# Kernel tuning notes

Measured on AMD Instinct MI355X. Metric: run time of the kernel, lower is better.

The kernel has to match this reference:

```python
import jax, jax.numpy as jnp
import numpy as np
import math

NUM_HEADS = 4
PH, PW = 8, 8

def setup_inputs() -> dict:
    key = jax.random.key(0)
    ks = jax.random.split(key, 12)
    B, C, H, W = 2, 128, 256, 256
    x = jax.random.normal(ks[0], (B, C, H, W), dtype=jnp.float32)
    mask = jax.random.uniform(ks[1], (B, 1, H, W), dtype=jnp.float32)
    s1 = 1.0 / math.sqrt(C)          # kaiming-ish scale for 1x1 convs
    s3 = 1.0 / math.sqrt(C * 9)      # 3x3 conv
    wq = jax.random.normal(ks[2], (C, C), dtype=jnp.float32) * s1
    bq = jax.random.normal(ks[3], (C,), dtype=jnp.float32) * 0.01
    wk = jax.random.normal(ks[4], (C, C), dtype=jnp.float32) * s1
    bk = jax.random.normal(ks[5], (C,), dtype=jnp.float32) * 0.01
    wv = jax.random.normal(ks[6], (C, C), dtype=jnp.float32) * s1
    bv = jax.random.normal(ks[7], (C,), dtype=jnp.float32) * 0.01
    wo = jax.random.normal(ks[8], (C, C, 3, 3), dtype=jnp.float32) * s3
    bo = jax.random.normal(ks[9], (C,), dtype=jnp.float32) * 0.01
    return {"x": x, "mask": mask, "wq": wq, "bq": bq, "wk": wk, "bk": bk,
            "wv": wv, "bv": bv, "wo": wo, "bo": bo}

def _conv1x1(x, w, b):
    # w: [O, I]; x: [B, C, H, W]
    return jnp.einsum('oc,bchw->bohw', w, x) + b[None, :, None, None]

def _window(t, b, heads, dph, out_h, out_w):
    # [B, C, H, W] -> [B, heads, out_h*out_w, dph*PH*PW]
    t = t.reshape(b, heads, dph, out_h, PH, out_w, PW)
    t = t.transpose(0, 1, 3, 5, 2, 4, 6)
    return t.reshape(b, heads, out_h * out_w, dph * PH * PW)

def reference(x, mask, wq, bq, wk, bk, wv, bv, wo, bo):
    b, c, h, w = x.shape
    heads = NUM_HEADS
    dph = c // heads
    out_h, out_w = h // PH, w // PW
    d = dph * PH * PW

    q = _window(_conv1x1(x, wq, bq), b, heads, dph, out_h, out_w)
    k = _window(_conv1x1(x, wk, bk), b, heads, dph, out_h, out_w)
    v = _window(_conv1x1(x, wv, bv), b, heads, dph, out_h, out_w)

    # NOTE: original torch code calls att.masked_fill(mask, -1e9) without
    # assignment (not in-place), so the mask has no effect on the output.
    att = jnp.einsum('bhqd,bhkd->bhqk', q, k) * (1.0 / math.sqrt(d))
    p = jax.nn.softmax(att, axis=-1)
    y = jnp.einsum('bhqk,bhkd->bhqd', p, v)

    # un-window: [B, heads, S, d] -> [B, C, H, W]
    y = y.reshape(b, heads, out_h, out_w, dph, PH, PW)
    y = y.transpose(0, 1, 4, 2, 5, 3, 6).reshape(b, c, h, w)

    # output: reflect-padded 3x3 conv + LeakyReLU(0.2)
    yp = jnp.pad(y, ((0, 0), (0, 0), (1, 1), (1, 1)), mode='reflect')
    out = jax.lax.conv_general_dilated(
        yp, wo, window_strides=(1, 1), padding='VALID',
        dimension_numbers=('NCHW', 'OIHW', 'NCHW')) + bo[None, :, None, None]
    return jnp.where(out > 0, out, 0.2 * out)
```

## Files before the change

kernel.cpp:

```cpp
#include <hip/hip_runtime.h>
#include <hip/hip_bf16.h>
#include <stdint.h>

typedef unsigned short u16;
typedef __attribute__((ext_vector_type(8))) short bf16x8;
typedef __attribute__((ext_vector_type(4))) short bf16x4;
typedef __attribute__((ext_vector_type(4))) float f32x4;
typedef __attribute__((ext_vector_type(4))) unsigned short u16x4;

__device__ __forceinline__ float bf2f(u16 u) {
  union { unsigned i; float f; } c; c.i = ((unsigned)u) << 16; return c.f;
}
__device__ __forceinline__ u16 f2bf(float f) {
  union { float f; unsigned i; } c; c.f = f;
  unsigned r = c.i + 0x7FFFu + ((c.i >> 16) & 1u);
  return (u16)(r >> 16);
}
__device__ __forceinline__ unsigned cvt_pk(float lo, float hi) {
  unsigned r;
  asm("v_cvt_pk_bf16_f32 %0, %1, %2" : "=v"(r) : "v"(lo), "v"(hi));
  return r;
}
__device__ __forceinline__ void gl2lds16(const u16* g, u16* l) {
  __builtin_amdgcn_global_load_lds(
      (const __attribute__((address_space(1))) unsigned int*)(uintptr_t)g,
      (__attribute__((address_space(3))) unsigned int*)(uintptr_t)l,
      16, 0, 0);
}

__global__ void k_prep(const float* __restrict__ wo, const float* __restrict__ wq,
                       const float* __restrict__ wk, const float* __restrict__ wv,
                       u16* __restrict__ WT, u16* __restrict__ WQKV) {
  int i = blockIdx.x * 256 + threadIdx.x;
  if (i < 9 * 128 * 128) {
    int c = i & 127;
    int o = (i >> 7) & 127;
    int tap = i >> 14;
    WT[i] = f2bf(wo[((o * 128 + c) * 3 + tap / 3) * 3 + tap % 3]);
  } else {
    int j = i - 9 * 128 * 128;
    if (j < 3 * 16384) {
      int sel = j >> 14, rest = j & 16383;
      const float* w = sel == 0 ? wq : (sel == 1 ? wk : wv);
      WQKV[j] = f2bf(w[rest]);
    }
  }
}

__global__ __launch_bounds__(256) void k_qkv(
    const float* __restrict__ x, const u16* __restrict__ WQKV,
    const float* __restrict__ bq, const float* __restrict__ bk,
    const float* __restrict__ bv,
    u16* __restrict__ Q, u16* __restrict__ K, u16* __restrict__ V) {
  const int sel = blockIdx.y;
  const int blk = blockIdx.x;
  const int b = blk >> 9;
  const int t = blk & 511;
  const int th = t & 31, tw = t >> 5;
  const int h0 = th * 8, w0 = tw * 16;
  const int s0 = th * 32 + tw * 2;
  const int tid = threadIdx.x, lane = tid & 63, wid = tid >> 6;
  const int wr = wid >> 1, wc = wid & 1;
  const int g = lane >> 4, l15 = lane & 15;

  __shared__ u16 Xt[128 * 136];
  u16* Ot = Xt;

  #pragma unroll
  for (int j = 0; j < 4; ++j) {
    int lin = j * 256 + tid;
    int c2 = lin >> 4;
    int ci = lin & 15;
    int c = c2 * 2;
    int lh = ci >> 1, lw8 = (ci & 1) * 8;
    const float* s0p = x + (size_t)b * 8388608 + (size_t)c * 65536 + (h0 + lh) * 256 + w0 + lw8;
    const float* s1p = s0p + 65536;
    float4 a0 = *(const float4*)s0p;
    float4 a1 = *(const float4*)(s0p + 4);
    float4 c0 = *(const float4*)s1p;
    float4 c1 = *(const float4*)(s1p + 4);
    int px = ci * 8;
    int ch = c >> 3;
    int chp = (ch & 8) | ((ch & 7) ^ (ci & 7));
    unsigned* dst = (unsigned*)&Xt[px * 136 + chp * 8 + (c & 7)];
    dst[0 * 68] = cvt_pk(a0.x, c0.x);
    dst[1 * 68] = cvt_pk(a0.y, c0.y);
    dst[2 * 68] = cvt_pk(a0.z, c0.z);
    dst[3 * 68] = cvt_pk(a0.w, c0.w);
    dst[4 * 68] = cvt_pk(a1.x, c1.x);
    dst[5 * 68] = cvt_pk(a1.y, c1.y);
    dst[6 * 68] = cvt_pk(a1.z, c1.z);
    dst[7 * 68] = cvt_pk(a1.w, c1.w);
  }
  __syncthreads();

  const u16* w = WQKV + sel * 16384;
  const float* bias = sel == 0 ? bq : (sel == 1 ? bk : bv);
  u16* qkv = sel == 0 ? Q : (sel == 1 ? K : V);

  f32x4 acc[4][4] = {};
  #pragma unroll
  for (int k0 = 0; k0 < 128; k0 += 32) {
    bf16x8 a[4], bb[4];
    #pragma unroll
    for (int m = 0; m < 4; ++m) {
      int o = wr * 64 + m * 16 + l15;
      a[m] = *(const bf16x8*)(w + o * 128 + k0 + g * 8);
    }
    #pragma unroll
    for (int n = 0; n < 4; ++n) {
      int p = wc * 64 + n * 16 + l15;
      int ch = (k0 >> 3) + g;
      int chp = (ch & 8) | ((ch & 7) ^ ((p >> 3) & 7));
      bb[n] = *(const bf16x8*)&Xt[p * 136 + chp * 8];
    }
    #pragma unroll
    for (int m = 0; m < 4; ++m)
      #pragma unroll
      for (int n = 0; n < 4; ++n)
        acc[m][n] = __builtin_amdgcn_mfma_f32_16x16x32_bf16(a[m], bb[n], acc[m][n], 0, 0, 0);
  }

  float4 bias4[4];
  #pragma unroll
  for (int m = 0; m < 4; ++m)
    bias4[m] = *(const float4*)&bias[wr * 64 + m * 16 + g * 4];

  __syncthreads();
  #pragma unroll
  for (int m = 0; m < 4; ++m) {
    int o0 = wr * 64 + m * 16 + g * 4;
    #pragma unroll
    for (int n = 0; n < 4; ++n) {
      int p = wc * 64 + n * 16 + l15;
      unsigned r0 = cvt_pk(acc[m][n][0] + bias4[m].x, acc[m][n][1] + bias4[m].y);
      unsigned r1 = cvt_pk(acc[m][n][2] + bias4[m].z, acc[m][n][3] + bias4[m].w);
      unsigned* dp = (unsigned*)&Ot[p * 136 + o0];
      dp[0] = r0; dp[1] = r1;
    }
  }
  __syncthreads();
  #pragma unroll
  for (int it = 0; it < 8; ++it) {
    int head = it >> 1, s2 = it & 1;
    int pixw = tid >> 2;
    int dphc = tid & 3;
    int pl = (pixw >> 3) * 16 + s2 * 8 + (pixw & 7);
    bf16x8 vv = *(const bf16x8*)&Ot[pl * 136 + head * 32 + dphc * 8];
    size_t gaddr = ((size_t)((b * 4 + head) * 1024 + s0 + s2)) * 2048 + pixw * 32 + dphc * 8;
    *(bf16x8*)(qkv + gaddr) = vv;
  }
}

__global__ __launch_bounds__(256) void k_qk(const u16* __restrict__ Q,
                                            const u16* __restrict__ K,
                                            float* __restrict__ ATT) {
  const int bh = blockIdx.x & 7;
  const int tile = blockIdx.x >> 3;
  const int tm = tile & 7, tn = tile >> 3;
  const int row0 = tm * 128, col0 = tn * 128;
  const int tid = threadIdx.x, lane = tid & 63, wid = tid >> 6;
  const int wr = wid >> 1, wc = wid & 1;
  __shared__ u16 As[128 * 32];
  __shared__ u16 Bs[128 * 32];
  const u16* Ab = Q + (size_t)bh * 1024 * 2048 + (size_t)row0 * 2048;
  const u16* Bb = K + (size_t)bh * 1024 * 2048 + (size_t)col0 * 2048;
  f32x4 acc[4][4] = {};
  const int lr = lane >> 2, lc = lane & 3;
  const int scs = lc ^ ((lr >> 1) & 3);
  const int rsw = ((lane & 15) >> 1) & 3;

  for (int k0 = 0; k0 < 2048; k0 += 32) {
    __syncthreads();
    const u16* s0 = Ab + (size_t)(wid * 16 + lr) * 2048 + k0 + scs * 8;
    gl2lds16(s0, &As[wid * 512]);
    gl2lds16(s0 + (size_t)64 * 2048, &As[2048 + wid * 512]);
    const u16* s1 = Bb + (size_t)(wid * 16 + lr) * 2048 + k0 + scs * 8;
    gl2lds16(s1, &Bs[wid * 512]);
    gl2lds16(s1 + (size_t)64 * 2048, &Bs[2048 + wid * 512]);
    asm volatile("s_waitcnt vmcnt(0)" ::: "memory");
    __syncthreads();
    bf16x8 a[4], bb[4];
    const int g = lane >> 4;
    const int chp = (g ^ rsw) * 8;
    #pragma unroll
    for (int m = 0; m < 4; ++m)
      a[m] = *(const bf16x8*)&As[(wr * 64 + m * 16 + (lane & 15)) * 32 + chp];
    #pragma unroll
    for (int n = 0; n < 4; ++n)
      bb[n] = *(const bf16x8*)&Bs[(wc * 64 + n * 16 + (lane & 15)) * 32 + chp];
    #pragma unroll
    for (int m = 0; m < 4; ++m)
      #pragma unroll
      for (int n = 0; n < 4; ++n)
        acc[m][n] = __builtin_amdgcn_mfma_f32_16x16x32_bf16(a[m], bb[n], acc[m][n], 0, 0, 0);
  }
  const float scale = 0.02209708691207961f;
  float* out = ATT + (size_t)bh * 1024 * 1024;
  #pragma unroll
  for (int m = 0; m < 4; ++m) {
    int r = row0 + wr * 64 + m * 16 + ((lane >> 4) << 2);
    #pragma unroll
    for (int n = 0; n < 4; ++n) {
      int cc = col0 + wc * 64 + n * 16 + (lane & 15);
      #pragma unroll
      for (int j = 0; j < 4; ++j)
        out[(size_t)(r + j) * 1024 + cc] = acc[m][n][j] * scale;
    }
  }
}

__global__ __launch_bounds__(256) void k_vt(const u16* __restrict__ V,
                                            u16* __restrict__ VT) {
  const int bh = blockIdx.y;
  const int ts = blockIdx.x & 7, td = blockIdx.x >> 3;
  const int s0 = ts * 128, d0 = td * 128;
  const int tid = threadIdx.x;
  __shared__ u16 T[128 * 128];
  const u16* Vb = V + (size_t)bh * 1024 * 2048 + (size_t)s0 * 2048 + d0;

  #pragma unroll
  for (int pass = 0; pass < 8; ++pass) {
    int r = pass * 16 + (tid >> 4);
    int c8 = (tid & 15) * 8;
    union { uint4 u; u16 e[8]; } d;
    d.u = *(const uint4*)(Vb + (size_t)r * 2048 + c8);
    int chunk = (r >> 3) ^ ((c8 >> 3) & 15);
    u16* dst = &T[0];
    #pragma unroll
    for (int e = 0; e < 8; ++e)
      dst[(c8 + e) * 128 + chunk * 8 + (r & 7)] = d.e[e];
  }
  __syncthreads();
  u16* VTb = VT + (size_t)bh * 2048 * 1024 + (size_t)d0 * 1024 + s0;
  #pragma unroll
  for (int pass = 0; pass < 8; ++pass) {
    int rd = pass * 16 + (tid >> 4);
    int c8 = (tid & 15) * 8;
    int chunk = (c8 >> 3) ^ ((rd >> 3) & 15);
    bf16x8 v = *(const bf16x8*)&T[rd * 128 + chunk * 8];
    *(bf16x8*)(VTb + (size_t)rd * 1024 + c8) = v;
  }
}

__global__ __launch_bounds__(256) void k_softmax(const float* __restrict__ ATT,
                                                 u16* __restrict__ P) {
  const int row = blockIdx.x;
  const float* a = ATT + (size_t)row * 1024;
  const int tid = threadIdx.x;
  float4 v = *(const float4*)(a + tid * 4);
  float mx = fmaxf(fmaxf(v.x, v.y), fmaxf(v.z, v.w));
  #pragma unroll
  for (int off = 32; off; off >>= 1) mx = fmaxf(mx, __shfl_xor(mx, off, 64));
  __shared__ float red[8];
  if ((tid & 63) == 0) red[tid >> 6] = mx;
  __syncthreads();
  mx = fmaxf(fmaxf(red[0], red[1]), fmaxf(red[2], red[3]));
  float e0 = __expf(v.x - mx), e1 = __expf(v.y - mx);
  float e2 = __expf(v.z - mx), e3 = __expf(v.w - mx);
  float s = e0 + e1 + e2 + e3;
  #pragma unroll
  for (int off = 32; off; off >>= 1) s += __shfl_xor(s, off, 64);
  if ((tid & 63) == 0) red[4 + (tid >> 6)] = s;
  __syncthreads();
  s = red[4] + red[5] + red[6] + red[7];
  float inv = 1.0f / s;
  u16x4 o = { f2bf(e0 * inv), f2bf(e1 * inv), f2bf(e2 * inv), f2bf(e3 * inv) };
  *(u16x4*)(P + (size_t)row * 1024 + tid * 4) = o;
}

__global__ __launch_bounds__(256) void k_pv(const u16* __restrict__ P,
                                            const u16* __restrict__ VT,
                                            u16* __restrict__ Yn) {
  const int bh = blockIdx.x & 7;
  const int tile = blockIdx.x >> 3;
  const int tm = tile & 7, tn = tile >> 3;
  const int row0 = tm * 128, col0 = tn * 128;
  const int tid = threadIdx.x, lane = tid & 63, wid = tid >> 6;
  const int wr = wid >> 1, wc = wid & 1;
  __shared__ __align__(16) u16 smem[17408];
  u16* As = smem;
  u16* Bs = smem + 4096;
  u16* Ot = smem;
  const u16* Pb = P + (size_t)bh * 1024 * 1024 + (size_t)row0 * 1024;
  const u16* VTb = VT + (size_t)bh * 2048 * 1024 + (size_t)col0 * 1024;
  f32x4 acc[4][4] = {};
  const int lr = lane >> 2, lc = lane & 3;
  const int scs = lc ^ ((lr >> 1) & 3);
  const int rsw = ((lane & 15) >> 1) & 3;

  for (int k0 = 0; k0 < 1024; k0 += 32) {
    __syncthreads();
    const u16* s0 = Pb + (size_t)(wid * 16 + lr) * 1024 + k0 + scs * 8;
    gl2lds16(s0, &As[wid * 512]);
    gl2lds16(s0 + (size_t)64 * 1024, &As[2048 + wid * 512]);
    const u16* s1 = VTb + (size_t)(wid * 16 + lr) * 1024 + k0 + scs * 8;
    gl2lds16(s1, &Bs[wid * 512]);
    gl2lds16(s1 + (size_t)64 * 1024, &Bs[2048 + wid * 512]);
    asm volatile("s_waitcnt vmcnt(0)" ::: "memory");
    __syncthreads();
    bf16x8 a[4], bb[4];
    const int g = lane >> 4;
    const int chp = (g ^ rsw) * 8;
    #pragma unroll
    for (int m = 0; m < 4; ++m)
      a[m] = *(const bf16x8*)&As[(wr * 64 + m * 16 + (lane & 15)) * 32 + chp];
    #pragma unroll
    for (int n = 0; n < 4; ++n)
      bb[n] = *(const bf16x8*)&Bs[(wc * 64 + n * 16 + (lane & 15)) * 32 + chp];
    #pragma unroll
    for (int m = 0; m < 4; ++m)
      #pragma unroll
      for (int n = 0; n < 4; ++n)
        acc[m][n] = __builtin_amdgcn_mfma_f32_16x16x32_bf16(a[m], bb[n], acc[m][n], 0, 0, 0);
  }

  __syncthreads();
  #pragma unroll
  for (int m = 0; m < 4; ++m) {
    int r0 = wr * 64 + m * 16 + ((lane >> 4) << 2);
    #pragma unroll
    for (int n = 0; n < 4; ++n) {
      int dv = wc * 64 + n * 16 + (lane & 15);
      #pragma unroll
      for (int j = 0; j < 4; ++j)
        Ot[(r0 + j) * 136 + dv] = f2bf(acc[m][n][j]);
    }
  }
  __syncthreads();
  const int b = bh >> 2, head = bh & 3;
  const int pixw0 = tn * 4;
  #pragma unroll
  for (int it = 0; it < 8; ++it) {
    int ci = it * 256 + tid;
    int sl = ci >> 4;
    int pxl = (ci >> 2) & 3;
    int dc = ci & 3;
    bf16x8 vv = *(const bf16x8*)&Ot[sl * 136 + pxl * 32 + dc * 8];
    int s = row0 + sl, oh = s >> 5, ow = s & 31;
    int pixw = pixw0 + pxl, ph = pixw >> 3, pw = pixw & 7;
    int h = oh * 8 + ph, w2 = ow * 8 + pw;
    size_t gaddr = (((size_t)(b * 256 + h) * 256) + w2) * 128 + head * 32 + dc * 8;
    *(bf16x8*)(Yn + gaddr) = vv;
  }
}

__global__ __launch_bounds__(512, 2) void k_conv(const u16* __restrict__ Yn,
                                                 const u16* __restrict__ WT,
                                                 const float* __restrict__ bo,
                                                 float* __restrict__ out) {
  const int wgid = blockIdx.x;
  const int r7 = wgid & 7;
  const int b = (r7 >> 2) & 1;
  const int w0 = ((r7 >> 1) & 1) * 128;
  const int h0 = ((r7 & 1) * 32 + (wgid >> 3)) * 4;
  const int tid = threadIdx.x, lane = tid & 63, wid = tid >> 6;
  const int wo_ = wid & 1;
  const int wh = wid >> 1;
  const int g = lane >> 4, l15 = lane & 15;
  __shared__ u16 S[6][136 * 64];
  __shared__ u16 WTl[2][8192];
  f32x4 acc[4][8] = {};

  auto stageS = [&](int chalf) {
    for (int g5 = wid; g5 < 102; g5 += 8) {
      int rowi = g5 / 17, grp = g5 % 17;
      int rg = grp * 8 + (lane >> 3);
      int chunk = lane & 7;
      int row = h0 + rowi - 1;
      row = row < 0 ? 1 : (row > 255 ? 254 : row);
      int wsrc = w0 - 1 + rg;
      wsrc = wsrc < 0 ? 1 : (wsrc > 255 ? 254 : wsrc);
      const u16* src = Yn + ((size_t)(b * 256 + row) * 256 + wsrc) * 128 + chalf * 64
                         + ((chunk ^ (rg & 7)) * 8);
      gl2lds16(src, &S[rowi][grp * 512]);
    }
  };
  auto stageWT = [&](int chalf, int tap, int nb) {
    #pragma unroll
    for (int r2 = 0; r2 < 2; ++r2) {
      int g5 = wid + r2 * 8;
      int orow = g5 * 8 + (lane >> 3);
      int csrc = (lane & 7) ^ (lane >> 3);
      const u16* src = WT + ((size_t)tap * 128 + orow) * 128 + chalf * 64 + csrc * 8;
      gl2lds16(src, &WTl[nb][g5 * 512]);
    }
  };

  int buf = 0;
  stageS(0);
  stageWT(0, 0, 0);
  asm volatile("s_waitcnt vmcnt(0)" ::: "memory");
  __syncthreads();

  #pragma unroll
  for (int chalf = 0; chalf < 2; ++chalf) {
    if (chalf) {
      __syncthreads();
      stageS(1);
      stageWT(1, 0, buf ^ 1);
      asm volatile("s_waitcnt vmcnt(0)" ::: "memory");
      __syncthreads();
      buf ^= 1;
    }
    #pragma unroll
    for (int ky = 0; ky < 3; ++ky) {
      #pragma unroll
      for (int kx = 0; kx < 3; ++kx) {
        const int tap = ky * 3 + kx;
        const bool hasNext = (tap < 8);
        if (hasNext) stageWT(chalf, tap + 1, buf ^ 1);
        bf16x8 areg[2][4];
        #pragma unroll
        for (int ckh = 0; ckh < 2; ++ckh)
          #pragma unroll
          for (int m = 0; m < 4; ++m) {
            int o = wo_ * 64 + m * 16 + l15;
            int cc2 = ((ckh << 2) + g) ^ (o & 7);
            areg[ckh][m] = *(const bf16x8*)&WTl[buf][o * 64 + cc2 * 8];
          }
        #pragma unroll
        for (int ckh = 0; ckh < 2; ++ckh) {
          #pragma unroll
          for (int nh = 0; nh < 2; ++nh) {
            bf16x8 bb[4];
            #pragma unroll
            for (int n4 = 0; n4 < 4; ++n4) {
              int p = (nh * 4 + n4) * 16 + l15 + kx;
              int chunk = ((ckh << 2) + g) ^ (p & 7);
              bb[n4] = *(const bf16x8*)&S[wh + ky][p * 64 + chunk * 8];
            }
            #pragma unroll
            for (int m = 0; m < 4; ++m)
              #pragma unroll
              for (int n4 = 0; n4 < 4; ++n4)
                acc[m][nh * 4 + n4] = __builtin_amdgcn_mfma_f32_16x16x32_bf16(
                    areg[ckh][m], bb[n4], acc[m][nh * 4 + n4], 0, 0, 0);
          }
        }
        if (hasNext) {
          asm volatile("s_waitcnt vmcnt(0)" ::: "memory");
          __syncthreads();
          buf ^= 1;
        }
      }
    }
  }
  #pragma unroll
  for (int m = 0; m < 4; ++m) {
    int o0 = wo_ * 64 + m * 16 + (g << 2);
    #pragma unroll
    for (int n = 0; n < 8; ++n) {
      int p = n * 16 + l15;
      #pragma unroll
      for (int j = 0; j < 4; ++j) {
        int o = o0 + j;
        float v = acc[m][n][j] + bo[o];
        v = v > 0.f ? v : 0.2f * v;
        out[(((size_t)b * 128 + o) << 16) + ((h0 + wh) << 8) + w0 + p] = v;
      }
    }
  }
}

extern "C" void kernel_launch(void* const* d_in, const int* in_sizes, int n_in,
                              void* d_out, int out_size, void* d_ws, size_t ws_size,
                              hipStream_t stream) {
  const float* x  = (const float*)d_in[0];
  const float* wq = (const float*)d_in[2];
  const float* bq = (const float*)d_in[3];
  const float* wk = (const float*)d_in[4];
  const float* bk = (const float*)d_in[5];
  const float* wv = (const float*)d_in[6];
  const float* bv = (const float*)d_in[7];
  const float* wo = (const float*)d_in[8];
  const float* bo = (const float*)d_in[9];

  char* ws = (char*)d_ws;
  u16*   WT   = (u16*)(ws);
  u16*   WQKV = (u16*)(ws + (size_t)(512 << 10));
  u16*   Q   = (u16*)(ws + (size_t)(1  << 20));
  u16*   K   = (u16*)(ws + (size_t)(33 << 20));
  u16*   V   = (u16*)(ws + (size_t)(65 << 20));
  float* ATT = (float*)(ws + (size_t)(97 << 20));
  u16*   P   = (u16*)(ws + (size_t)(129 << 20));
  u16*   Yn  = (u16*)(ws + (size_t)(145 << 20));
  u16*   VT  = Q;
  float* outp = (float*)d_out;

  k_prep<<<768, 256, 0, stream>>>(wo, wq, wk, wv, WT, WQKV);
  k_qkv<<<dim3(1024, 3), 256, 0, stream>>>(x, WQKV, bq, bk, bv, Q, K, V);
  k_qk<<<512, 256, 0, stream>>>(Q, K, ATT);
  k_vt<<<dim3(128, 8), 256, 0, stream>>>(V, VT);
  k_softmax<<<8192, 256, 0, stream>>>(ATT, P);
  k_pv<<<1024, 256, 0, stream>>>(P, VT, Yn);
  k_conv<<<256, 512, 0, stream>>>(Yn, WT, bo, outp);
}
```

Baseline: 224.0 us.

## Load x tile once into registers and compute Q, K, V in one block

The QKV projection kernel previously launched three blocks per tile (one per Q/K/V), and each block reloaded and converted the same x tile through LDS. Now each block loads its x fragments straight from global memory into MFMA B-operand registers once and loops over the three weight matrices, cutting x reads by a factor of three and removing the LDS staging. The trade-offs are more registers held per thread (the bfrag array), a grid with a third as many blocks, and global loads that are scalar and strided rather than float4.

```diff
diff --git a/kernel.cpp b/kernel.cpp
--- a/kernel.cpp
+++ b/kernel.cpp
@@ -52,7 +52,6 @@
     const float* __restrict__ bq, const float* __restrict__ bk,
     const float* __restrict__ bv,
     u16* __restrict__ Q, u16* __restrict__ K, u16* __restrict__ V) {
-  const int sel = blockIdx.y;
   const int blk = blockIdx.x;
   const int b = blk >> 9;
   const int t = blk & 511;
@@ -63,92 +62,74 @@
   const int wr = wid >> 1, wc = wid & 1;
   const int g = lane >> 4, l15 = lane & 15;
 
-  __shared__ u16 Xt[128 * 136];
-  u16* Ot = Xt;
-
-  #pragma unroll
-  for (int j = 0; j < 4; ++j) {
-    int lin = j * 256 + tid;
-    int c2 = lin >> 4;
-    int ci = lin & 15;
-    int c = c2 * 2;
-    int lh = ci >> 1, lw8 = (ci & 1) * 8;
-    const float* s0p = x + (size_t)b * 8388608 + (size_t)c * 65536 + (h0 + lh) * 256 + w0 + lw8;
-    const float* s1p = s0p + 65536;
-    float4 a0 = *(const float4*)s0p;
-    float4 a1 = *(const float4*)(s0p + 4);
-    float4 c0 = *(const float4*)s1p;
-    float4 c1 = *(const float4*)(s1p + 4);
-    int px = ci * 8;
-    int ch = c >> 3;
-    int chp = (ch & 8) | ((ch & 7) ^ (ci & 7));
-    unsigned* dst = (unsigned*)&Xt[px * 136 + chp * 8 + (c & 7)];
-    dst[0 * 68] = cvt_pk(a0.x, c0.x);
-    dst[1 * 68] = cvt_pk(a0.y, c0.y);
-    dst[2 * 68] = cvt_pk(a0.z, c0.z);
-    dst[3 * 68] = cvt_pk(a0.w, c0.w);
-    dst[4 * 68] = cvt_pk(a1.x, c1.x);
-    dst[5 * 68] = cvt_pk(a1.y, c1.y);
-    dst[6 * 68] = cvt_pk(a1.z, c1.z);
-    dst[7 * 68] = cvt_pk(a1.w, c1.w);
-  }
-  __syncthreads();
-
-  const u16* w = WQKV + sel * 16384;
-  const float* bias = sel == 0 ? bq : (sel == 1 ? bk : bv);
-  u16* qkv = sel == 0 ? Q : (sel == 1 ? K : V);
-
-  f32x4 acc[4][4] = {};
-  #pragma unroll
-  for (int k0 = 0; k0 < 128; k0 += 32) {
-    bf16x8 a[4], bb[4];
+  __shared__ u16 Ot[128 * 136];
+
+  bf16x8 bfrag[4][4];
+  {
+    const float* xb = x + (size_t)b * 8388608 + (size_t)(g * 8) * 65536
+                        + (h0 + wc * 4) * 256 + w0 + l15;
+    #pragma unroll
+    for (int ks = 0; ks < 4; ++ks)
+      #pragma unroll
+      for (int e2 = 0; e2 < 4; ++e2) {
+        const float* pa = xb + (size_t)(ks * 32 + e2 * 2) * 65536;
+        const float* pb = pa + 65536;
+        #pragma unroll
+        for (int n = 0; n < 4; ++n)
+          ((unsigned*)&bfrag[ks][n])[e2] = cvt_pk(pa[n * 256], pb[n * 256]);
+      }
+  }
+
+  for (int sel = 0; sel < 3; ++sel) {
+    const u16* w = WQKV + sel * 16384;
+    const float* bias = sel == 0 ? bq : (sel == 1 ? bk : bv);
+    u16* qkv = sel == 0 ? Q : (sel == 1 ? K : V);
+
+    f32x4 acc[4][4] = {};
+    #pragma unroll
+    for (int ks = 0; ks < 4; ++ks) {
+      bf16x8 a[4];
+      #pragma unroll
+      for (int m = 0; m < 4; ++m) {
+        int o = wr * 64 + m * 16 + l15;
+        a[m] = *(const bf16x8*)(w + o * 128 + ks * 32 + g * 8);
+      }
+      #pragma unroll
+      for (int m = 0; m < 4; ++m)
+        #pragma unroll
+        for (int n = 0; n < 4; ++n)
+          acc[m][n] = __builtin_amdgcn_mfma_f32_16x16x32_bf16(a[m], bfrag[ks][n], acc[m][n], 0, 0, 0);
+    }
+
+    float4 bias4[4];
+    #pragma unroll
+    for (int m = 0; m < 4; ++m)
+      bias4[m] = *(const float4*)&bias[wr * 64 + m * 16 + g * 4];
+
+    __syncthreads();
     #pragma unroll
     for (int m = 0; m < 4; ++m) {
-      int o = wr * 64 + m * 16 + l15;
-      a[m] = *(const bf16x8*)(w + o * 128 + k0 + g * 8);
-    }
-    #pragma unroll
-    for (int n = 0; n < 4; ++n) {
-      int p = wc * 64 + n * 16 + l15;
-      int ch = (k0 >> 3) + g;
-      int chp = (ch & 8) | ((ch & 7) ^ ((p >> 3) & 7));
-      bb[n] = *(const bf16x8*)&Xt[p * 136 + chp * 8];
-    }
-    #pragma unroll
-    for (int m = 0; m < 4; ++m)
-      #pragma unroll
-      for (int n = 0; n < 4; ++n)
-        acc[m][n] = __builtin_amdgcn_mfma_f32_16x16x32_bf16(a[m], bb[n], acc[m][n], 0, 0, 0);
-  }
-
-  float4 bias4[4];
-  #pragma unroll
-  for (int m = 0; m < 4; ++m)
-    bias4[m] = *(const float4*)&bias[wr * 64 + m * 16 + g * 4];
-
-  __syncthreads();
-  #pragma unroll
-  for (int m = 0; m < 4; ++m) {
-    int o0 = wr * 64 + m * 16 + g * 4;
-    #pragma unroll
-    for (int n = 0; n < 4; ++n) {
-      int p = wc * 64 + n * 16 + l15;
-      unsigned r0 = cvt_pk(acc[m][n][0] + bias4[m].x, acc[m][n][1] + bias4[m].y);
-      unsigned r1 = cvt_pk(acc[m][n][2] + bias4[m].z, acc[m][n][3] + bias4[m].w);
-      unsigned* dp = (unsigned*)&Ot[p * 136 + o0];
-      dp[0] = r0; dp[1] = r1;
-    }
-  }
-  __syncthreads();
-  #pragma unroll
-  for (int it = 0; it < 8; ++it) {
-    int head = it >> 1, s2 = it & 1;
-    int pixw = tid >> 2;
-    int dphc = tid & 3;
-    int pl = (pixw >> 3) * 16 + s2 * 8 + (pixw & 7);
-    bf16x8 vv = *(const bf16x8*)&Ot[pl * 136 + head * 32 + dphc * 8];
-    size_t gaddr = ((size_t)((b * 4 + head) * 1024 + s0 + s2)) * 2048 + pixw * 32 + dphc * 8;
-    *(bf16x8*)(qkv + gaddr) = vv;
+      int o0 = wr * 64 + m * 16 + g * 4;
+      #pragma unroll
+      for (int n = 0; n < 4; ++n) {
+        int p = wc * 64 + n * 16 + l15;
+        unsigned r0 = cvt_pk(acc[m][n][0] + bias4[m].x, acc[m][n][1] + bias4[m].y);
+        unsigned r1 = cvt_pk(acc[m][n][2] + bias4[m].z, acc[m][n][3] + bias4[m].w);
+        unsigned* dp = (unsigned*)&Ot[p * 136 + o0];
+        dp[0] = r0; dp[1] = r1;
+      }
+    }
+    __syncthreads();
+    #pragma unroll
+    for (int it = 0; it < 8; ++it) {
+      int head = it >> 1, s2 = it & 1;
+      int pixw = tid >> 2;
+      int dphc = tid & 3;
+      int pl = (pixw >> 3) * 16 + s2 * 8 + (pixw & 7);
+      bf16x8 vv = *(const bf16x8*)&Ot[pl * 136 + head * 32 + dphc * 8];
+      size_t gaddr = ((size_t)((b * 4 + head) * 1024 + s0 + s2)) * 2048 + pixw * 32 + dphc * 8;
+      *(bf16x8*)(qkv + gaddr) = vv;
+    }
   }
 }
 
@@ -489,7 +470,7 @@
   float* outp = (float*)d_out;
 
   k_prep<<<768, 256, 0, stream>>>(wo, wq, wk, wv, WT, WQKV);
-  k_qkv<<<dim3(1024, 3), 256, 0, stream>>>(x, WQKV, bq, bk, bv, Q, K, V);
+  k_qkv<<<1024, 256, 0, stream>>>(x, WQKV, bq, bk, bv, Q, K, V);
   k_qk<<<512, 256, 0, stream>>>(Q, K, ATT);
   k_vt<<<dim3(128, 8), 256, 0, stream>>>(V, VT);
   k_softmax<<<8192, 256, 0, stream>>>(ATT, P);
```

Measured after the change: 214.4 us. 1.04x faster.
